# Kernel optimization log

Hardware: AMD Instinct MI355X
Metric: run time of the kernel (lower is better)

Reference implementation:

```python
import jax, jax.numpy as jnp
import numpy as np

H = 300  # hidden size hardcoded in the module
VX = 32000
VY = 32000
NX, NY, B = 128, 128, 256


def setup_inputs() -> dict:
    key = jax.random.key(0)
    ks = jax.random.split(key, 10)
    s = 1.0 / np.sqrt(H)
    x = jax.random.randint(ks[0], (NX, B), 0, VX)
    y = jax.random.randint(ks[1], (NY, B), 0, VY)
    # padding_idx=0: zero the pad row of each embedding table
    enc_emb = jax.random.normal(ks[2], (VX, H), jnp.float32).at[0].set(0.0)
    encW = jax.random.uniform(ks[3], (H, H), jnp.float32, -s, s)
    encb = jax.random.uniform(ks[4], (H,), jnp.float32, -s, s)
    dec_emb = jax.random.normal(ks[5], (VY, H), jnp.float32).at[0].set(0.0)
    decW = jax.random.uniform(ks[6], (H, H), jnp.float32, -s, s)
    decb = jax.random.uniform(ks[7], (H,), jnp.float32, -s, s)
    outW = jax.random.uniform(ks[8], (VY, H), jnp.float32, -s, s)
    outb = jax.random.uniform(ks[9], (VY,), jnp.float32, -s, s)
    return {"x": x, "y": y, "enc_emb": enc_emb, "encW": encW, "encb": encb,
            "dec_emb": dec_emb, "decW": decW, "decb": decb,
            "outW": outW, "outb": outb}


def reference(x, y, enc_emb, encW, encb, dec_emb, decW, decb, outW, outb):
    # Encoder: Elman recurrence h = relu(e_x[i] + W h + b)
    e_x = enc_emb[x]                                  # [NX, B, H]
    h0 = jnp.zeros((x.shape[1], H), e_x.dtype)        # h=0 broadcast over batch

    def enc_step(h, ex):
        return jax.nn.relu(ex + h @ encW.T + encb), None

    h, _ = jax.lax.scan(enc_step, h0, e_x)

    # Decoder: teacher-forced recurrence with per-step mean cross-entropy
    e_y = dec_emb[y]                                  # [NY, B, H]

    def dec_step(h, inp):
        ey, tgt = inp
        h = jax.nn.relu(ey + h @ decW.T + decb)
        logits = h @ outW.T + outb                    # [B, VY]
        logp = jax.nn.log_softmax(logits, axis=-1)
        ce = -jnp.mean(jnp.take_along_axis(logp, tgt[:, None], axis=-1))
        return h, ce

    _, ces = jax.lax.scan(dec_step, h, (e_y[:-1], y[1:]))
    return jnp.sum(ces)
```

## Files before the change

kernel.cpp:

```cpp
#include <hip/hip_runtime.h>
#include <hip/hip_bf16.h>
#include <stdint.h>

typedef unsigned short u16;
typedef unsigned char u8;
typedef float f32x4 __attribute__((ext_vector_type(4)));
typedef float f32x2 __attribute__((ext_vector_type(2)));
typedef _Float16 f16x2 __attribute__((ext_vector_type(2)));
typedef _Float16 f16x8 __attribute__((ext_vector_type(8)));

#define H      300
#define KP     320
#define BATCH  256
#define NX     128
#define NY     128
#define VY     32000
#define NPAD   32768
#define MROWS  32512

#define OW8_OFF  0UL
#define OW8_BYTES ((unsigned long)NPAD * KP)
#define A8_OFF   (OW8_OFF + OW8_BYTES)
#define A8_BYTES ((unsigned long)MROWS * KP)
#define WTE_OFF  (A8_OFF + A8_BYTES)
#define WT_BYTES ((unsigned long)H * KP * 4)
#define WTD_OFF  (WTE_OFF + WT_BYTES)
#define SE_OFF   (WTD_OFF + WT_BYTES)
#define SE_BYTES ((unsigned long)MROWS * 4)

typedef const __attribute__((address_space(1))) char* gp_t;
typedef __attribute__((address_space(3))) char* lp_t;

__global__ __launch_bounds__(256) void k0_prep(const float* __restrict__ outW,
                                               const float* __restrict__ encW,
                                               const float* __restrict__ decW,
                                               u8* __restrict__ ow8,
                                               float* __restrict__ wte,
                                               float* __restrict__ wtd) {
    long id = (long)blockIdx.x * 256 + threadIdx.x;
    const long n1 = (long)NPAD * KP / 4;
    if (id < n1) {
        int v = (int)(id / 80), k4 = (int)(id % 80) * 4;
        float4 f = {0.f, 0.f, 0.f, 0.f};
        if (v < VY && k4 < H) f = *(const float4*)&outW[(long)v * H + k4];
        int w = __builtin_amdgcn_cvt_pk_fp8_f32(f.x, f.y, 0, false);
        w = __builtin_amdgcn_cvt_pk_fp8_f32(f.z, f.w, w, true);
        ((unsigned int*)ow8)[id] = (unsigned int)w;
        return;
    }
    long id2 = id - n1;
    if (id2 < (long)H * KP) {
        int k = (int)(id2 / KP), j = (int)(id2 % KP);
        wte[id2] = (j < H) ? encW[j * H + k] : 0.f;
        return;
    }
    id2 -= (long)H * KP;
    if (id2 < (long)H * KP) {
        int k = (int)(id2 / KP), j = (int)(id2 % KP);
        wtd[id2] = (j < H) ? decW[j * H + k] : 0.f;
    }
}

__global__ __launch_bounds__(960, 4) void k1_rnn(const int* __restrict__ x,
                                                 const int* __restrict__ y,
                                                 const float* __restrict__ enc_emb,
                                                 const float* __restrict__ dec_emb,
                                                 const float* __restrict__ encb,
                                                 const float* __restrict__ decb,
                                                 const float* __restrict__ wte,
                                                 const float* __restrict__ wtd,
                                                 u8* __restrict__ A8) {
    const int tid = threadIdx.x;
    const int s = tid / 320;
    const int j = tid - s * 320;
    const int b = blockIdx.x;

    __shared__ __align__(16) _Float16 hh[320];
    __shared__ float part[960];
    __shared__ __align__(4) u8 a8row[320];

    for (int i = tid; i < 320; i += 960) hh[i] = (_Float16)0.f;

    const bool comb = (tid < 320);
    const float be = (comb && j < H) ? encb[j] : 0.f;
    const float bd = (comb && j < H) ? decb[j] : 0.f;

    f16x2 w[52];
#pragma unroll
    for (int kk = 0; kk < 52; ++kk) {
        int k0 = 2 * (s * 52 + kk);
        float f0 = (k0 < H)     ? wte[k0 * KP + j]       : 0.f;
        float f1 = (k0 + 1 < H) ? wte[(k0 + 1) * KP + j] : 0.f;
        w[kk] = (f16x2){(_Float16)f0, (_Float16)f1};
    }

    int idx_n = x[BATCH + b];
    float e_cur = 0.f;
    if (comb && j < H) e_cur = enc_emb[(long)x[b] * H + j];
    __syncthreads();

    const f16x8* hb8 = (const f16x8*)&hh[s * 104];

    for (int t = 0; t < NX; ++t) {
        int idx_n2 = x[min(t + 2, NX - 1) * BATCH + b];
        float e_nx = 0.f;
        if (comb && j < H && t + 1 < NX) e_nx = enc_emb[(long)idx_n * H + j];

        float p0 = 0.f, p1 = 0.f;
#pragma unroll
        for (int i = 0; i < 13; ++i) {
            f16x8 hv = hb8[i];
            f16x2 a0 = {hv[0], hv[1]}, a1 = {hv[2], hv[3]};
            f16x2 a2 = {hv[4], hv[5]}, a3 = {hv[6], hv[7]};
            p0 = __builtin_amdgcn_fdot2(w[4 * i + 0], a0, p0, false);
            p1 = __builtin_amdgcn_fdot2(w[4 * i + 1], a1, p1, false);
            p0 = __builtin_amdgcn_fdot2(w[4 * i + 2], a2, p0, false);
            p1 = __builtin_amdgcn_fdot2(w[4 * i + 3], a3, p1, false);
        }
        part[tid] = p0 + p1;
        __syncthreads();
        if (comb) {
            float v = part[j] + part[320 + j] + part[640 + j] + be + e_cur;
            hh[j] = (_Float16)fmaxf(v, 0.f);
        }
        __syncthreads();
        e_cur = e_nx; idx_n = idx_n2;
    }

#pragma unroll
    for (int kk = 0; kk < 52; ++kk) {
        int k0 = 2 * (s * 52 + kk);
        float f0 = (k0 < H)     ? wtd[k0 * KP + j]       : 0.f;
        float f1 = (k0 + 1 < H) ? wtd[(k0 + 1) * KP + j] : 0.f;
        w[kk] = (f16x2){(_Float16)f0, (_Float16)f1};
    }

    idx_n = y[BATCH + b];
    e_cur = 0.f;
    if (comb && j < H) e_cur = dec_emb[(long)y[b] * H + j];

    for (int t = 0; t < NY - 1; ++t) {
        int idx_n2 = y[min(t + 2, NY - 1) * BATCH + b];
        float e_nx = 0.f;
        if (comb && j < H && t + 1 < NY - 1) e_nx = dec_emb[(long)idx_n * H + j];

        float p0 = 0.f, p1 = 0.f;
#pragma unroll
        for (int i = 0; i < 13; ++i) {
            f16x8 hv = hb8[i];
            f16x2 a0 = {hv[0], hv[1]}, a1 = {hv[2], hv[3]};
            f16x2 a2 = {hv[4], hv[5]}, a3 = {hv[6], hv[7]};
            p0 = __builtin_amdgcn_fdot2(w[4 * i + 0], a0, p0, false);
            p1 = __builtin_amdgcn_fdot2(w[4 * i + 1], a1, p1, false);
            p0 = __builtin_amdgcn_fdot2(w[4 * i + 2], a2, p0, false);
            p1 = __builtin_amdgcn_fdot2(w[4 * i + 3], a3, p1, false);
        }
        part[tid] = p0 + p1;
        __syncthreads();
        if (comb) {
            float v = part[j] + part[320 + j] + part[640 + j] + bd + e_cur;
            v = fmaxf(v, 0.f);
            hh[j] = (_Float16)v;
            int pk = __builtin_amdgcn_cvt_pk_fp8_f32(v, v, 0, false);
            a8row[j] = (u8)(pk & 0xff);
        }
        __syncthreads();
        if (tid < 80)
            ((unsigned int*)(A8 + (long)(t * BATCH + b) * KP))[tid] =
                ((const unsigned int*)a8row)[tid];
        e_cur = e_nx; idx_n = idx_n2;
    }
}

__global__ __launch_bounds__(256, 2) void k2_gemm(const u8* __restrict__ A8,
                                                  const u8* __restrict__ OW8,
                                                  const float* __restrict__ outb,
                                                  float* __restrict__ sumexp) {
    const int tid = threadIdx.x;
    const int lane = tid & 63, wave = tid >> 6;
    const int lane16 = lane & 15, quad = lane >> 4;
    const int cg = blockIdx.x & 7;
    const int rb = blockIdx.x >> 3;
    const int colbase = cg * 4096;

    __shared__ u8 Bld[4 * 8192];
    __shared__ float rowsum[64];
    if (tid < 64) rowsum[tid] = 0.f;
    __syncthreads();

    u8* wbuf = &Bld[wave * 8192];

    long a[4][10];
    {
        const u8* abase = A8 + ((long)rb * 64 + lane16) * KP + quad * 8;
#pragma unroll
        for (int rt = 0; rt < 4; ++rt)
#pragma unroll
            for (int ks = 0; ks < 10; ++ks)
                a[rt][ks] = *(const long*)(abase + rt * 16 * KP + ks * 32);
    }

    auto stage = [&](int ct3, int ks3, int slot) {
        int colb = colbase + ct3 * 256 + wave * 64;
        const u8* g0 = OW8 + (long)(colb + (lane >> 1)) * KP + ks3 * 32 + (lane & 1) * 16;
        u8* l0 = wbuf + slot * 2048 + lane * 16;
        __builtin_amdgcn_global_load_lds((gp_t)g0, (lp_t)l0, 16, 0, 0);
        __builtin_amdgcn_global_load_lds((gp_t)(g0 + 32 * KP), (lp_t)(l0 + 1024), 16, 0, 0);
    };

    stage(0, 0, 0); stage(0, 1, 1); stage(0, 2, 2);

    float rsum[16];
#pragma unroll
    for (int i = 0; i < 16; ++i) rsum[i] = 0.f;

    for (int ct = 0; ct < 16; ++ct) {
        f32x4 acc[4][4];
#pragma unroll
        for (int p = 0; p < 4; ++p)
#pragma unroll
            for (int q = 0; q < 4; ++q) acc[p][q] = (f32x4){0.f, 0.f, 0.f, 0.f};

#pragma unroll
        for (int ks = 0; ks < 10; ++ks) {
            int s_ct = (ks + 3 < 10) ? ct : ct + 1;
            int s_ks = (ks + 3 < 10) ? (ks + 3) : (ks - 7);
            if (s_ct > 15) { s_ct = 15; s_ks = 9; }
            stage(s_ct, s_ks, (ct * 10 + ks + 3) & 3);

            __builtin_amdgcn_s_waitcnt(0x0F76);

            const u8* rb8 = wbuf + ((ct * 10 + ks) & 3) * 2048;
            long bfr[4];
#pragma unroll
            for (int tc = 0; tc < 4; ++tc)
                bfr[tc] = *(const long*)&rb8[(tc * 16 + lane16) * 32 + quad * 8];
#pragma unroll
            for (int rt = 0; rt < 4; ++rt)
#pragma unroll
                for (int tc = 0; tc < 4; ++tc)
                    acc[rt][tc] = __builtin_amdgcn_mfma_f32_16x16x32_fp8_fp8(
                        a[rt][ks], bfr[tc], acc[rt][tc], 0, 0, 0);
        }

        int cb = colbase + ct * 256 + wave * 64;
#pragma unroll
        for (int tc = 0; tc < 4; ++tc) {
            int v = cb + tc * 16 + lane16;
            bool valid = v < VY;
            float ob = valid ? outb[v] : 0.f;
#pragma unroll
            for (int rt = 0; rt < 4; ++rt)
#pragma unroll
                for (int i = 0; i < 4; ++i) {
                    float lg = acc[rt][tc][i] + ob;
                    if (valid) rsum[rt * 4 + i] += __expf(lg);
                }
        }
    }

#pragma unroll
    for (int m = 1; m < 16; m <<= 1)
#pragma unroll
        for (int i = 0; i < 16; ++i) rsum[i] += __shfl_xor(rsum[i], m, 64);
    if (lane16 == 0) {
#pragma unroll
        for (int rt = 0; rt < 4; ++rt)
#pragma unroll
            for (int i = 0; i < 4; ++i)
                atomicAdd(&rowsum[rt * 16 + quad * 4 + i], rsum[rt * 4 + i]);
    }
    __syncthreads();
    if (tid < 64) atomicAdd(&sumexp[(long)rb * 64 + tid], rowsum[tid]);
}

__global__ __launch_bounds__(256) void k3_ce(const u8* __restrict__ A8,
                                             const u8* __restrict__ OW8,
                                             const float* __restrict__ outb,
                                             const float* __restrict__ sumexp,
                                             const int* __restrict__ y,
                                             float* __restrict__ out) {
    const int wave = threadIdx.x >> 6, lane = threadIdx.x & 63;
    const int r = blockIdx.x * 4 + wave;
    const int t = r >> 8, b = r & 255;
    const int tgt = y[(t + 1) * BATCH + b];
    const unsigned int* ar = (const unsigned int*)(A8 + (long)r * KP);
    const unsigned int* wr_ = (const unsigned int*)(OW8 + (long)tgt * KP);
    float s = 0.f;
#pragma unroll
    for (int i = 0; i < 2; ++i) {
        int c = i * 64 + lane;
        if (c < 80) {
            unsigned int a4 = ar[c], w4 = wr_[c];
            f32x2 al = __builtin_amdgcn_cvt_pk_f32_fp8(a4, false);
            f32x2 ah = __builtin_amdgcn_cvt_pk_f32_fp8(a4, true);
            f32x2 wl = __builtin_amdgcn_cvt_pk_f32_fp8(w4, false);
            f32x2 wh = __builtin_amdgcn_cvt_pk_f32_fp8(w4, true);
            s += al[0] * wl[0] + al[1] * wl[1] + ah[0] * wh[0] + ah[1] * wh[1];
        }
    }
#pragma unroll
    for (int m = 1; m < 64; m <<= 1) s += __shfl_xor(s, m, 64);
    __shared__ float part[4];
    if (lane == 0) part[wave] = logf(sumexp[r]) - (s + outb[tgt]);
    __syncthreads();
    if (threadIdx.x == 0) {
        float tot = part[0] + part[1] + part[2] + part[3];
        atomicAdd(out, tot * (1.0f / 256.0f));
    }
}

extern "C" void kernel_launch(void* const* d_in, const int* in_sizes, int n_in,
                              void* d_out, int out_size, void* d_ws, size_t ws_size,
                              hipStream_t stream) {
    (void)in_sizes; (void)n_in; (void)out_size; (void)ws_size;
    const int*   x       = (const int*)d_in[0];
    const int*   y       = (const int*)d_in[1];
    const float* enc_emb = (const float*)d_in[2];
    const float* encW    = (const float*)d_in[3];
    const float* encb    = (const float*)d_in[4];
    const float* dec_emb = (const float*)d_in[5];
    const float* decW    = (const float*)d_in[6];
    const float* decb    = (const float*)d_in[7];
    const float* outW    = (const float*)d_in[8];
    const float* outb    = (const float*)d_in[9];

    char* ws = (char*)d_ws;
    u8* ow8  = (u8*)(ws + OW8_OFF);
    u8* A8   = (u8*)(ws + A8_OFF);
    float* wte    = (float*)(ws + WTE_OFF);
    float* wtd    = (float*)(ws + WTD_OFF);
    float* sumexp = (float*)(ws + SE_OFF);

    hipMemsetAsync(sumexp, 0, SE_BYTES, stream);
    hipMemsetAsync(d_out, 0, sizeof(float), stream);

    long n0 = (long)NPAD * KP / 4 + 2L * H * KP;
    k0_prep<<<(int)((n0 + 255) / 256), 256, 0, stream>>>(outW, encW, decW, ow8, wte, wtd);
    k1_rnn<<<256, 960, 0, stream>>>(x, y, enc_emb, dec_emb, encb, decb, wte, wtd, A8);
    k2_gemm<<<508 * 8, 256, 0, stream>>>(A8, ow8, outb, sumexp);
    k3_ce<<<8128, 256, 0, stream>>>(A8, ow8, outb, sumexp, y, (float*)d_out);
}
```

Measured before the change: 1.193 ms.

## Pre-swizzle fp8 output weights into MFMA fragment order, drop LDS staging

The prep kernel now writes the fp8 output-projection weights in a layout that matches the MFMA B-fragment order: 64-column blocks, then k-slices, then 16-column tiles. The GEMM kernel then loads each B fragment straight from global memory with coalesced 8-byte loads, replacing the global-to-LDS staging pipeline and its waitcnts. The CE kernel is changed to index the swizzled layout. This frees LDS and removes staging overhead, but global-load latency is no longer hidden by explicit multi-stage prefetch.

```diff
diff --git a/kernel.cpp b/kernel.cpp
--- a/kernel.cpp
+++ b/kernel.cpp
@@ -18,9 +18,10 @@
 #define NPAD   32768
 #define MROWS  32512
 
-#define OW8_OFF  0UL
-#define OW8_BYTES ((unsigned long)NPAD * KP)
-#define A8_OFF   (OW8_OFF + OW8_BYTES)
+
+#define OWS_OFF  0UL
+#define OWS_BYTES ((unsigned long)NPAD * KP)
+#define A8_OFF   (OWS_OFF + OWS_BYTES)
 #define A8_BYTES ((unsigned long)MROWS * KP)
 #define WTE_OFF  (A8_OFF + A8_BYTES)
 #define WT_BYTES ((unsigned long)H * KP * 4)
@@ -28,13 +29,10 @@
 #define SE_OFF   (WTD_OFF + WT_BYTES)
 #define SE_BYTES ((unsigned long)MROWS * 4)
 
-typedef const __attribute__((address_space(1))) char* gp_t;
-typedef __attribute__((address_space(3))) char* lp_t;
-
 __global__ __launch_bounds__(256) void k0_prep(const float* __restrict__ outW,
                                                const float* __restrict__ encW,
                                                const float* __restrict__ decW,
-                                               u8* __restrict__ ow8,
+                                               u8* __restrict__ ows,
                                                float* __restrict__ wte,
                                                float* __restrict__ wtd) {
     long id = (long)blockIdx.x * 256 + threadIdx.x;
@@ -45,7 +43,9 @@
         if (v < VY && k4 < H) f = *(const float4*)&outW[(long)v * H + k4];
         int w = __builtin_amdgcn_cvt_pk_fp8_f32(f.x, f.y, 0, false);
         w = __builtin_amdgcn_cvt_pk_fp8_f32(f.z, f.w, w, true);
-        ((unsigned int*)ow8)[id] = (unsigned int)w;
+        long dst = (long)(v >> 6) * 20480 + (k4 >> 5) * 2048 + ((v >> 4) & 3) * 512
+                 + (v & 15) * 8 + ((k4 >> 3) & 3) * 128 + (k4 & 7);
+        *(unsigned int*)(ows + dst) = (unsigned int)w;
         return;
     }
     long id2 = id - n1;
@@ -173,7 +173,7 @@
 }
 
 __global__ __launch_bounds__(256, 2) void k2_gemm(const u8* __restrict__ A8,
-                                                  const u8* __restrict__ OW8,
+                                                  const u8* __restrict__ OWS,
                                                   const float* __restrict__ outb,
                                                   float* __restrict__ sumexp) {
     const int tid = threadIdx.x;
@@ -183,13 +183,10 @@
     const int rb = blockIdx.x >> 3;
     const int colbase = cg * 4096;
 
-    __shared__ u8 Bld[4 * 8192];
     __shared__ float rowsum[64];
     if (tid < 64) rowsum[tid] = 0.f;
     __syncthreads();
 
-    u8* wbuf = &Bld[wave * 8192];
-
     long a[4][10];
     {
         const u8* abase = A8 + ((long)rb * 64 + lane16) * KP + quad * 8;
@@ -200,21 +197,14 @@
                 a[rt][ks] = *(const long*)(abase + rt * 16 * KP + ks * 32);
     }
 
-    auto stage = [&](int ct3, int ks3, int slot) {
-        int colb = colbase + ct3 * 256 + wave * 64;
-        const u8* g0 = OW8 + (long)(colb + (lane >> 1)) * KP + ks3 * 32 + (lane & 1) * 16;
-        u8* l0 = wbuf + slot * 2048 + lane * 16;
-        __builtin_amdgcn_global_load_lds((gp_t)g0, (lp_t)l0, 16, 0, 0);
-        __builtin_amdgcn_global_load_lds((gp_t)(g0 + 32 * KP), (lp_t)(l0 + 1024), 16, 0, 0);
-    };
-
-    stage(0, 0, 0); stage(0, 1, 1); stage(0, 2, 2);
+    const u8* wb = OWS + (long)(cg * 64 + wave) * 20480 + lane * 8;
 
     float rsum[16];
 #pragma unroll
     for (int i = 0; i < 16; ++i) rsum[i] = 0.f;
 
     for (int ct = 0; ct < 16; ++ct) {
+        const u8* ctp = wb + (long)ct * 4 * 20480;
         f32x4 acc[4][4];
 #pragma unroll
         for (int p = 0; p < 4; ++p)
@@ -223,18 +213,11 @@
 
 #pragma unroll
         for (int ks = 0; ks < 10; ++ks) {
-            int s_ct = (ks + 3 < 10) ? ct : ct + 1;
-            int s_ks = (ks + 3 < 10) ? (ks + 3) : (ks - 7);
-            if (s_ct > 15) { s_ct = 15; s_ks = 9; }
-            stage(s_ct, s_ks, (ct * 10 + ks + 3) & 3);
-
-            __builtin_amdgcn_s_waitcnt(0x0F76);
-
-            const u8* rb8 = wbuf + ((ct * 10 + ks) & 3) * 2048;
+            const u8* p = ctp + ks * 2048;
             long bfr[4];
 #pragma unroll
             for (int tc = 0; tc < 4; ++tc)
-                bfr[tc] = *(const long*)&rb8[(tc * 16 + lane16) * 32 + quad * 8];
+                bfr[tc] = *(const long*)(p + tc * 512);
 #pragma unroll
             for (int rt = 0; rt < 4; ++rt)
 #pragma unroll
@@ -275,7 +258,7 @@
 }
 
 __global__ __launch_bounds__(256) void k3_ce(const u8* __restrict__ A8,
-                                             const u8* __restrict__ OW8,
+                                             const u8* __restrict__ OWS,
                                              const float* __restrict__ outb,
                                              const float* __restrict__ sumexp,
                                              const int* __restrict__ y,
@@ -284,20 +267,24 @@
     const int r = blockIdx.x * 4 + wave;
     const int t = r >> 8, b = r & 255;
     const int tgt = y[(t + 1) * BATCH + b];
-    const unsigned int* ar = (const unsigned int*)(A8 + (long)r * KP);
-    const unsigned int* wr_ = (const unsigned int*)(OW8 + (long)tgt * KP);
     float s = 0.f;
-#pragma unroll
-    for (int i = 0; i < 2; ++i) {
-        int c = i * 64 + lane;
-        if (c < 80) {
-            unsigned int a4 = ar[c], w4 = wr_[c];
-            f32x2 al = __builtin_amdgcn_cvt_pk_f32_fp8(a4, false);
-            f32x2 ah = __builtin_amdgcn_cvt_pk_f32_fp8(a4, true);
-            f32x2 wl = __builtin_amdgcn_cvt_pk_f32_fp8(w4, false);
-            f32x2 wh = __builtin_amdgcn_cvt_pk_f32_fp8(w4, true);
-            s += al[0] * wl[0] + al[1] * wl[1] + ah[0] * wh[0] + ah[1] * wh[1];
-        }
+    if (lane < 40) {
+        unsigned long long av = *(const unsigned long long*)(A8 + (long)r * KP + lane * 8);
+        long wdst = (long)(tgt >> 6) * 20480 + (lane >> 2) * 2048
+                  + ((tgt >> 4) & 3) * 512 + (tgt & 15) * 8 + (lane & 3) * 128;
+        unsigned long long wv = *(const unsigned long long*)(OWS + wdst);
+        unsigned int a4 = (unsigned int)av, a4h = (unsigned int)(av >> 32);
+        unsigned int w4 = (unsigned int)wv, w4h = (unsigned int)(wv >> 32);
+        f32x2 al = __builtin_amdgcn_cvt_pk_f32_fp8(a4, false);
+        f32x2 ah = __builtin_amdgcn_cvt_pk_f32_fp8(a4, true);
+        f32x2 wl = __builtin_amdgcn_cvt_pk_f32_fp8(w4, false);
+        f32x2 wh = __builtin_amdgcn_cvt_pk_f32_fp8(w4, true);
+        s += al[0] * wl[0] + al[1] * wl[1] + ah[0] * wh[0] + ah[1] * wh[1];
+        al = __builtin_amdgcn_cvt_pk_f32_fp8(a4h, false);
+        ah = __builtin_amdgcn_cvt_pk_f32_fp8(a4h, true);
+        wl = __builtin_amdgcn_cvt_pk_f32_fp8(w4h, false);
+        wh = __builtin_amdgcn_cvt_pk_f32_fp8(w4h, true);
+        s += al[0] * wl[0] + al[1] * wl[1] + ah[0] * wh[0] + ah[1] * wh[1];
     }
 #pragma unroll
     for (int m = 1; m < 64; m <<= 1) s += __shfl_xor(s, m, 64);
@@ -326,7 +313,7 @@
     const float* outb    = (const float*)d_in[9];
 
     char* ws = (char*)d_ws;
-    u8* ow8  = (u8*)(ws + OW8_OFF);
+    u8* ows  = (u8*)(ws + OWS_OFF);
     u8* A8   = (u8*)(ws + A8_OFF);
     float* wte    = (float*)(ws + WTE_OFF);
     float* wtd    = (float*)(ws + WTD_OFF);
@@ -336,8 +323,8 @@
     hipMemsetAsync(d_out, 0, sizeof(float), stream);
 
     long n0 = (long)NPAD * KP / 4 + 2L * H * KP;
-    k0_prep<<<(int)((n0 + 255) / 256), 256, 0, stream>>>(outW, encW, decW, ow8, wte, wtd);
+    k0_prep<<<(int)((n0 + 255) / 256), 256, 0, stream>>>(outW, encW, decW, ows, wte, wtd);
     k1_rnn<<<256, 960, 0, stream>>>(x, y, enc_emb, dec_emb, encb, decb, wte, wtd, A8);
-    k2_gemm<<<508 * 8, 256, 0, stream>>>(A8, ow8, outb, sumexp);
-    k3_ce<<<8128, 256, 0, stream>>>(A8, ow8, outb, sumexp, y, (float*)d_out);
-}
+    k2_gemm<<<508 * 8, 256, 0, stream>>>(A8, ows, outb, sumexp);
+    k3_ce<<<8128, 256, 0, stream>>>(A8, ows, outb, sumexp, y, (float*)d_out);
+}
```

Result: faster. 1.039 ms (-12.9%).
